# Kernel tuning notes

Measured on AMD Instinct MI355X. Metric: run time of the kernel, lower is better.

The kernel has to match this reference:

```python
import jax, jax.numpy as jnp
import numpy as np

B, N = 8, 2000                  # images, proposals per image
NUM_CLASSES = 91                # incl. background (class 0)
IMG_H, IMG_W = 800, 1333
SCORE_THRESH = 0.05
NMS_THRESH = 0.5
DETS_PER_IMG = 100
PRE_NMS_TOPK = 2048             # fixed-size cap on NMS candidates (jit-static)
MIN_SIZE = 0.01
WX, WY, WW, WH = 10.0, 10.0, 5.0, 5.0   # BoxCoder weights
BBOX_XFORM_CLIP = float(np.log(1000.0 / 16.0))


def setup_inputs() -> dict:
    key = jax.random.key(0)
    k1, k2, k3, k4 = jax.random.split(key, 4)
    # valid proposal boxes (x1,y1,x2,y2) inside the image
    ctr = jax.random.uniform(k1, (B, N, 2)) * jnp.array([IMG_W, IMG_H], jnp.float32)
    wh = jax.random.uniform(k2, (B, N, 2), minval=8.0, maxval=256.0)
    proposals = jnp.concatenate([ctr - 0.5 * wh, ctr + 0.5 * wh], axis=-1)
    class_logits = jax.random.normal(k3, (B * N, NUM_CLASSES)) * 2.0
    box_regression = jax.random.normal(k4, (B * N, NUM_CLASSES * 4)) * 0.2
    return {"class_logits": class_logits, "box_regression": box_regression,
            "proposals": proposals}


def _decode(reg, boxes):
    # reg: [N, C, 4] deltas, boxes: [N, 4] proposals -> [N, C, 4] decoded
    w = boxes[:, 2] - boxes[:, 0]
    h = boxes[:, 3] - boxes[:, 1]
    cx = boxes[:, 0] + 0.5 * w
    cy = boxes[:, 1] + 0.5 * h
    dx = reg[..., 0] / WX
    dy = reg[..., 1] / WY
    dw = jnp.minimum(reg[..., 2] / WW, BBOX_XFORM_CLIP)
    dh = jnp.minimum(reg[..., 3] / WH, BBOX_XFORM_CLIP)
    pcx = dx * w[:, None] + cx[:, None]
    pcy = dy * h[:, None] + cy[:, None]
    pw = jnp.exp(dw) * w[:, None]
    ph = jnp.exp(dh) * h[:, None]
    return jnp.stack([pcx - 0.5 * pw, pcy - 0.5 * ph,
                      pcx + 0.5 * pw, pcy + 0.5 * ph], axis=-1)


def _box_iou(a, b):
    # a: [K,4], b: [K,4] -> [K,K]
    area_a = (a[:, 2] - a[:, 0]) * (a[:, 3] - a[:, 1])
    area_b = (b[:, 2] - b[:, 0]) * (b[:, 3] - b[:, 1])
    lt = jnp.maximum(a[:, None, :2], b[None, :, :2])
    rb = jnp.minimum(a[:, None, 2:], b[None, :, 2:])
    wh = jnp.clip(rb - lt, 0.0)
    inter = wh[..., 0] * wh[..., 1]
    return inter / (area_a[:, None] + area_b[None, :] - inter)


def _postprocess_image(boxes, scores):
    # boxes: [N, C, 4] decoded, scores: [N, C] softmax probs
    boxes = jnp.stack([jnp.clip(boxes[..., 0], 0.0, IMG_W),
                       jnp.clip(boxes[..., 1], 0.0, IMG_H),
                       jnp.clip(boxes[..., 2], 0.0, IMG_W),
                       jnp.clip(boxes[..., 3], 0.0, IMG_H)], axis=-1)
    # drop background class 0, flatten to per-(proposal,class) candidates
    boxes_fg = boxes[:, 1:, :].reshape(-1, 4)            # [N*(C-1), 4]
    scores_fg = scores[:, 1:].reshape(-1)
    labels_fg = jnp.broadcast_to(jnp.arange(1, NUM_CLASSES, dtype=jnp.int32),
                                 (N, NUM_CLASSES - 1)).reshape(-1)
    ws = boxes_fg[:, 2] - boxes_fg[:, 0]
    hs = boxes_fg[:, 3] - boxes_fg[:, 1]
    valid = (scores_fg > SCORE_THRESH) & (ws >= MIN_SIZE) & (hs >= MIN_SIZE)
    # fixed-size pre-NMS top-K (masked-out candidates sorted last)
    _, top_idx = jax.lax.top_k(jnp.where(valid, scores_fg, -1.0), PRE_NMS_TOPK)
    cand_boxes = boxes_fg[top_idx]
    cand_scores = scores_fg[top_idx]
    cand_labels = labels_fg[top_idx]
    cand_valid = valid[top_idx]
    # class-wise (batched) NMS via per-class coordinate offset
    offset = cand_labels.astype(cand_boxes.dtype) * (jnp.max(cand_boxes) + 1.0)
    iou = _box_iou(cand_boxes + offset[:, None], cand_boxes + offset[:, None])
    idx = jnp.arange(PRE_NMS_TOPK)

    def body(i, keep):  # greedy suppression in score order
        sup = (iou[i] > NMS_THRESH) & keep[i] & (idx > i)
        return keep & ~sup

    keep = jax.lax.fori_loop(0, PRE_NMS_TOPK, body, cand_valid)
    out_scores, out_idx = jax.lax.top_k(jnp.where(keep, cand_scores, -1.0),
                                        DETS_PER_IMG)
    return cand_boxes[out_idx], out_scores, cand_labels[out_idx]


def reference(class_logits, box_regression, proposals):
    logits = class_logits.reshape(B, N, NUM_CLASSES)
    reg = box_regression.reshape(B, N, NUM_CLASSES, 4)
    pred_boxes = jax.vmap(_decode)(reg, proposals)          # [B, N, C, 4]
    pred_scores = jax.nn.softmax(logits, axis=-1)           # [B, N, C]
    boxes, scores, labels = jax.vmap(_postprocess_image)(pred_boxes, pred_scores)
    return boxes, scores, labels
```

## Files before the change

kernel.cpp:

```cpp
#include <hip/hip_runtime.h>
#include <cstdint>
#include <cstddef>

#define NIMG   8
#define NPROP  2000
#define NCLS   91
#define NFG    90
#define NROW   (NIMG * NPROP)
#define TOPK   2048
#define DETS   100
#define CKCAP  32768
#define KREGS  12
#define CLSCAP 512

#define IMG_Wf 1333.0f
#define IMG_Hf 800.0f
#define SCORE_TH 0.05f
#define MINSZ    0.01f
#define NMS_TH   0.5f
#define CLIPV    4.135166556742356f
#define ORD_NEG1 0x407FFFFFu
#define PADKEY   (((ull)ORD_NEG1 << 32) | 0xFFFFFFFFull)

typedef unsigned long long ull;

static const size_t OFF_CNT    = 0;
static const size_t OFF_VBM    = 4096;
static const size_t OFF_CK     = 262144;
static const size_t OFF_CBOX   = OFF_CK    + (size_t)NIMG*CKCAP*8;
static const size_t OFF_CSCOR  = OFF_CBOX  + (size_t)NIMG*TOPK*16;
static const size_t OFF_CLAB   = OFF_CSCOR + (size_t)NIMG*TOPK*4;
static const size_t OFF_CLSBOX = OFF_CLAB  + (size_t)NIMG*TOPK*4;
static const size_t OFF_CLSAR  = OFF_CLSBOX+ (size_t)NIMG*TOPK*16;
static const size_t OFF_CLSSX  = OFF_CLSAR + (size_t)NIMG*TOPK*4;
static const size_t OFF_CLSCNT = OFF_CLSSX + (size_t)NIMG*TOPK*4;
static const size_t OFF_CLSOFF = OFF_CLSCNT+ (size_t)NIMG*96*4;
static const size_t OFF_KCLS   = OFF_CLSOFF+ (size_t)NIMG*96*4;

__device__ __forceinline__ unsigned ford(float f) {
    unsigned u = __float_as_uint(f);
    return (u & 0x80000000u) ? ~u : (u | 0x80000000u);
}
__device__ __forceinline__ float fordinv(unsigned x) {
    return (x & 0x80000000u) ? __uint_as_float(x & 0x7FFFFFFFu)
                             : __uint_as_float(~x);
}

__device__ __forceinline__ float4 decode_clip(float4 p, float4 r) {
    float w  = __fsub_rn(p.z, p.x);
    float h  = __fsub_rn(p.w, p.y);
    float cx = __fadd_rn(p.x, __fmul_rn(0.5f, w));
    float cy = __fadd_rn(p.y, __fmul_rn(0.5f, h));
    float dx = __fdiv_rn(r.x, 10.0f);
    float dy = __fdiv_rn(r.y, 10.0f);
    float dw = fminf(__fdiv_rn(r.z, 5.0f), CLIPV);
    float dh = fminf(__fdiv_rn(r.w, 5.0f), CLIPV);
    float pcx = __fadd_rn(__fmul_rn(dx, w), cx);
    float pcy = __fadd_rn(__fmul_rn(dy, h), cy);
    float pw  = __fmul_rn(expf(dw), w);
    float ph  = __fmul_rn(expf(dh), h);
    float x1 = __fsub_rn(pcx, __fmul_rn(0.5f, pw));
    float y1 = __fsub_rn(pcy, __fmul_rn(0.5f, ph));
    float x2 = __fadd_rn(pcx, __fmul_rn(0.5f, pw));
    float y2 = __fadd_rn(pcy, __fmul_rn(0.5f, ph));
    float4 o;
    o.x = fminf(fmaxf(x1, 0.0f), IMG_Wf);
    o.y = fminf(fmaxf(y1, 0.0f), IMG_Hf);
    o.z = fminf(fmaxf(x2, 0.0f), IMG_Wf);
    o.w = fminf(fmaxf(y2, 0.0f), IMG_Hf);
    return o;
}

__device__ __forceinline__ void wl_phase(ull& a, ull& b, int l, int base,
                                         int k, int jmax) {
    bool desc = ((base & k) == 0);
    for (int j = jmax; j >= 2; j >>= 1) {
        int pl = l ^ (j >> 1);
        bool lower = ((base & j) == 0);
        ull pa = __shfl(a, pl), pb = __shfl(b, pl);
        bool km = (desc == lower);
        ull na = km ? (a > pa ? a : pa) : (a < pa ? a : pa);
        ull nb = km ? (b > pb ? b : pb) : (b < pb ? b : pb);
        a = na; b = nb;
    }
    ull mx = a > b ? a : b, mn = a > b ? b : a;
    a = desc ? mx : mn; b = desc ? mn : mx;
}

__global__ __launch_bounds__(1024) void kA(const float* __restrict__ logits,
                                           const float* __restrict__ reg,
                                           const float* __restrict__ props,
                                           ull* __restrict__ ck,
                                           int* __restrict__ cntv,
                                           ull* __restrict__ vbm2) {
    int warp = threadIdx.x >> 6;
    int lane = threadIdx.x & 63;
    int row  = blockIdx.x * 16 + warp;
    int b = row / NPROP;
    int n = row - b * NPROP;
    const float* lrow = logits + (size_t)row * NCLS;

    float xa = lrow[lane];
    float xb = (lane < 27) ? lrow[64 + lane] : -INFINITY;
    float mx = fmaxf(xa, xb);
    #pragma unroll
    for (int o = 32; o; o >>= 1) mx = fmaxf(mx, __shfl_xor(mx, o));
    float ea = expf(__fsub_rn(xa, mx));
    float eb = (lane < 27) ? expf(__fsub_rn(xb, mx)) : 0.0f;
    float s  = __fadd_rn(ea, eb);
    #pragma unroll
    for (int o = 32; o; o >>= 1) s = __fadd_rn(s, __shfl_xor(s, o));

    const float4 p = *reinterpret_cast<const float4*>(props + (size_t)row * 4);

    __shared__ int sCnt[32];
    __shared__ int sExc[32];
    __shared__ int sBase;

    ull rowmask[2];
    bool validA[2];
    ull keyA[2];
    #pragma unroll
    for (int it = 0; it < 2; ++it) {
        int c = (it == 0) ? (1 + lane) : (65 + lane);
        bool active = (it == 0) ? true : (lane < 26);
        bool valid = false;
        ull key = 0;
        if (active) {
            float lg = lrow[c];
            float score = __fdiv_rn(expf(__fsub_rn(lg, mx)), s);
            float4 r4 = *reinterpret_cast<const float4*>(
                reg + ((size_t)row * NCLS + c) * 4);
            float4 bx = decode_clip(p, r4);
            float bw = __fsub_rn(bx.z, bx.x);
            float bh = __fsub_rn(bx.w, bx.y);
            valid = (score > SCORE_TH) && (bw >= MINSZ) && (bh >= MINSZ);
            int offidx = n * NFG + (c - 1);
            key = ((ull)ford(score) << 32) |
                  (ull)(0xFFFFFFFFu - (unsigned)offidx);
        }
        ull bal = __ballot(valid);
        rowmask[it] = bal;
        validA[it] = valid;
        keyA[it] = key;
        if (lane == 0) sCnt[warp * 2 + it] = __popcll(bal);
    }
    __syncthreads();
    if (warp == 0) {
        int c = (lane < 32) ? sCnt[lane] : 0;
        int p2 = c;
        #pragma unroll
        for (int o = 1; o < 32; o <<= 1) {
            int v = __shfl_up(p2, o);
            if (lane >= o) p2 += v;
        }
        if (lane == 31) sBase = atomicAdd(&cntv[b * 64], p2);
        if (lane < 32) sExc[lane] = p2 - c;
    }
    __syncthreads();
    int base = sBase;
    #pragma unroll
    for (int it = 0; it < 2; ++it) {
        if (validA[it]) {
            int slot = base + sExc[warp * 2 + it] +
                       __popcll(rowmask[it] & ((1ull << lane) - 1ull));
            if (slot < CKCAP)
                ck[(size_t)b * CKCAP + slot] = keyA[it];
        }
    }
    if (lane == 0) {
        vbm2[(size_t)row * 2]     = rowmask[0];
        vbm2[(size_t)row * 2 + 1] = rowmask[1];
    }
}

__global__ __launch_bounds__(1024) void kB(const ull* __restrict__ ck,
                                           const int* __restrict__ cntv,
                                           const ull* __restrict__ vbm2,
                                           const float* __restrict__ reg,
                                           const float* __restrict__ props,
                                           float4* __restrict__ cbox,
                                           float* __restrict__ cscore,
                                           int* __restrict__ clabel,
                                           float4* __restrict__ clsbox,
                                           float* __restrict__ clsarea,
                                           int* __restrict__ clssidx,
                                           int* __restrict__ clscnt,
                                           int* __restrict__ clsoff) {
    int b = blockIdx.x;
    int tid = threadIdx.x;
    int lane = tid & 63, warp = tid >> 6;
    __shared__ ull sk[TOPK];
    __shared__ unsigned histw[16 * 256];
    __shared__ unsigned wtot4[4];
    __shared__ ull sP;
    __shared__ int sRem, sCnt, sDone;
    __shared__ float sMax[16];
    __shared__ float sM1;
    __shared__ int rex[NPROP];
    __shared__ int wsum[16];
    __shared__ ull clsbm[NFG * 33];
    __shared__ unsigned wpfx[NFG * 33];
    __shared__ int ccnt[96], coff[96];

    int cnt = cntv[b * 64];
    if (cnt > CKCAP) cnt = CKCAP;
    const ull* K = ck + (size_t)b * CKCAP;

    if (cnt >= TOPK) {
        ull kreg[KREGS];
        #pragma unroll
        for (int r = 0; r < KREGS; ++r) {
            int i = tid + (r << 10);
            kreg[r] = (i < cnt) ? K[i] : 0ull;
        }
        ull P = 0; int rem = TOPK;
        for (int pass = 7; pass >= 0; --pass) {
            int sh = pass * 8;
            *reinterpret_cast<uint4*>(&histw[tid * 4]) = make_uint4(0, 0, 0, 0);
            __syncthreads();
            ull pmask = (pass == 7) ? 0ull : (~0ull << (sh + 8));
            unsigned* hw = &histw[warp << 8];
            #pragma unroll
            for (int r = 0; r < KREGS; ++r) {
                int i = tid + (r << 10);
                if (i < cnt && (kreg[r] & pmask) == P)
                    atomicAdd(&hw[(unsigned)(kreg[r] >> sh) & 255u], 1u);
            }
            for (int i = (KREGS << 10) + tid; i < cnt; i += 1024) {
                ull k2 = K[i];
                if ((k2 & pmask) == P)
                    atomicAdd(&hw[(unsigned)(k2 >> sh) & 255u], 1u);
            }
            __syncthreads();
            unsigned x = 0, pfx = 0;
            if (tid < 256) {
                int d = 255 - tid;
                #pragma unroll
                for (int w = 0; w < 16; ++w) x += histw[(w << 8) + d];
                pfx = x;
                #pragma unroll
                for (int o = 1; o < 64; o <<= 1) {
                    unsigned v = __shfl_up(pfx, o);
                    if (lane >= o) pfx += v;
                }
                if (lane == 63) wtot4[tid >> 6] = pfx;
            }
            __syncthreads();
            if (tid < 256) {
                int d = 255 - tid;
                int ws = tid >> 6;
                unsigned add = 0;
                if (ws > 0) add += wtot4[0];
                if (ws > 1) add += wtot4[1];
                if (ws > 2) add += wtot4[2];
                unsigned pi   = pfx + add;
                unsigned excl = pi - x;
                if (x && excl < (unsigned)rem && pi >= (unsigned)rem) {
                    sP = P | ((ull)(unsigned)d << sh);
                    int nr = rem - (int)excl;
                    sRem = nr;
                    sDone = ((int)x == nr) ? 1 : 0;
                }
            }
            __syncthreads();
            P = sP; rem = sRem;
            if (sDone) break;
        }
        if (tid == 0) sCnt = 0;
        __syncthreads();
        #pragma unroll
        for (int r = 0; r < KREGS; ++r) {
            int i = tid + (r << 10);
            bool sel = (i < cnt) && (kreg[r] >= P);
            ull bal = __ballot(sel);
            int cw = __popcll(bal);
            if (cw) {
                int ldr = __ffsll((long long)bal) - 1;
                int bw = 0;
                if (lane == ldr) bw = atomicAdd(&sCnt, cw);
                bw = __shfl(bw, ldr);
                if (sel) {
                    int pos = bw + __popcll(bal & ((1ull << lane) - 1ull));
                    if (pos < TOPK) sk[pos] = kreg[r];
                }
            }
        }
        for (int i = (KREGS << 10) + tid; i < cnt; i += 1024) {
            ull k2 = K[i];
            bool sel = (k2 >= P);
            ull bal = __ballot(sel);
            int cw = __popcll(bal);
            if (cw) {
                int ldr = __ffsll((long long)bal) - 1;
                int bw = 0;
                if (lane == ldr) bw = atomicAdd(&sCnt, cw);
                bw = __shfl(bw, ldr);
                if (sel) {
                    int pos = bw + __popcll(bal & ((1ull << lane) - 1ull));
                    if (pos < TOPK) sk[pos] = k2;
                }
            }
        }
        __syncthreads();
        int fc = sCnt;
        for (int i = fc + tid; i < TOPK; i += 1024) sk[i] = PADKEY;
    } else {
        for (int i = tid; i < cnt; i += 1024) sk[i] = K[i];
        int F = TOPK - cnt;
        const ull* V = vbm2 + (size_t)b * NPROP * 2;
        int r0 = 2 * tid, r1 = r0 + 1;
        int v0 = 0, v1 = 0;
        if (r0 < NPROP) v0 = NFG - __popcll(V[r0 * 2]) - __popcll(V[r0 * 2 + 1]);
        if (r1 < NPROP) v1 = NFG - __popcll(V[r1 * 2]) - __popcll(V[r1 * 2 + 1]);
        int s2 = v0 + v1;
        int pfx = s2;
        #pragma unroll
        for (int o = 1; o < 64; o <<= 1) {
            int t = __shfl_up(pfx, o);
            if (lane >= o) pfx += t;
        }
        if (lane == 63) wsum[warp] = pfx;
        __syncthreads();
        if (tid == 0) {
            int a = 0;
            for (int w = 0; w < 16; ++w) { int t = wsum[w]; wsum[w] = a; a += t; }
        }
        __syncthreads();
        int excl = pfx - s2 + wsum[warp];
        if (r0 < NPROP) rex[r0] = excl;
        if (r1 < NPROP) rex[r1] = excl + v0;
        __syncthreads();
        for (int r = tid; r < NPROP; r += 1024) {
            int e = rex[r];
            if (e < F) {
                ull m0 = V[r * 2], m1 = V[r * 2 + 1];
                int rank = e;
                ull inv = ~m0;
                while (inv && rank < F) {
                    int cb = __builtin_ctzll(inv); inv &= inv - 1;
                    unsigned idx = (unsigned)(r * NFG + cb);
                    sk[cnt + rank] = ((ull)ORD_NEG1 << 32) | (ull)(0xFFFFFFFFu - idx);
                    ++rank;
                }
                inv = (~m1) & ((1ull << 26) - 1ull);
                while (inv && rank < F) {
                    int cb = __builtin_ctzll(inv); inv &= inv - 1;
                    unsigned idx = (unsigned)(r * NFG + 64 + cb);
                    sk[cnt + rank] = ((ull)ORD_NEG1 << 32) | (ull)(0xFFFFFFFFu - idx);
                    ++rank;
                }
            }
        }
    }
    __syncthreads();

    {
        int ebase = warp * 128 + lane * 2;
        ulonglong2 v = *reinterpret_cast<ulonglong2*>(&sk[ebase]);
        ull a = v.x, bb = v.y;
        #pragma unroll
        for (int k = 2; k <= 128; k <<= 1)
            wl_phase(a, bb, lane, ebase, k, (k >> 1) < 64 ? (k >> 1) : 64);
        v.x = a; v.y = bb;
        *reinterpret_cast<ulonglong2*>(&sk[ebase]) = v;
        for (int k = 256; k <= TOPK; k <<= 1) {
            for (int j = k >> 1; j >= 128; j >>= 1) {
                __syncthreads();
                int i = ((tid & ~(j - 1)) << 1) | (tid & (j - 1));
                int ij = i | j;
                ull x1 = sk[i], x2 = sk[ij];
                bool descSeg = ((i & k) == 0);
                if ((x1 < x2) == descSeg) { sk[i] = x2; sk[ij] = x1; }
            }
            __syncthreads();
            v = *reinterpret_cast<ulonglong2*>(&sk[ebase]);
            a = v.x; bb = v.y;
            wl_phase(a, bb, lane, ebase, k, 64);
            v.x = a; v.y = bb;
            *reinterpret_cast<ulonglong2*>(&sk[ebase]) = v;
        }
    }
    __syncthreads();

    float lmax = 0.0f;
    float4 myb[2]; int myl[2]; float mys[2]; bool vkA[2];
    #pragma unroll
    for (int r = 0; r < 2; ++r) {
        int sidx = tid + r * 1024;
        ull k = sk[sidx];
        unsigned idx = 0xFFFFFFFFu - (unsigned)(k & 0xFFFFFFFFu);
        float score = fordinv((unsigned)(k >> 32));
        int n = (int)(idx / NFG), c = (int)(idx % NFG);
        int row = b * NPROP + n;
        float4 p  = *reinterpret_cast<const float4*>(props + (size_t)row * 4);
        float4 r4 = *reinterpret_cast<const float4*>(
            reg + ((size_t)row * NCLS + (c + 1)) * 4);
        float4 bx = decode_clip(p, r4);
        myb[r] = bx; myl[r] = c + 1; mys[r] = score;
        vkA[r] = (((unsigned)(k >> 32)) != ORD_NEG1);
        lmax = fmaxf(lmax, fmaxf(fmaxf(bx.x, bx.y), fmaxf(bx.z, bx.w)));
    }
    #pragma unroll
    for (int o = 32; o; o >>= 1) lmax = fmaxf(lmax, __shfl_xor(lmax, o));
    if ((tid & 63) == 0) sMax[tid >> 6] = lmax;
    __syncthreads();
    if (tid == 0) {
        float v = sMax[0];
        for (int i = 1; i < 16; ++i) v = fmaxf(v, sMax[i]);
        sM1 = __fadd_rn(v, 1.0f);
    }
    __syncthreads();
    float m1 = sM1;
    float4 obA[2]; float arA[2];
    #pragma unroll
    for (int r = 0; r < 2; ++r) {
        int sidx = tid + r * 1024;
        float off = __fmul_rn((float)myl[r], m1);
        float4 ob;
        ob.x = __fadd_rn(myb[r].x, off);
        ob.y = __fadd_rn(myb[r].y, off);
        ob.z = __fadd_rn(myb[r].z, off);
        ob.w = __fadd_rn(myb[r].w, off);
        float area = __fmul_rn(__fsub_rn(ob.z, ob.x), __fsub_rn(ob.w, ob.y));
        obA[r] = ob; arA[r] = area;
        int g = b * TOPK + sidx;
        cbox[g] = myb[r]; cscore[g] = mys[r]; clabel[g] = myl[r];
    }

    for (int i = tid; i < NFG * 33; i += 1024) clsbm[i] = 0ull;
    __syncthreads();
    #pragma unroll
    for (int r = 0; r < 2; ++r) {
        int sidx = tid + (r << 10);
        if (vkA[r])
            atomicOr(&clsbm[(myl[r] - 1) * 33 + (sidx >> 6)], 1ull << (sidx & 63));
    }
    __syncthreads();
    if (tid < NFG) {
        unsigned run = 0;
        for (int w = 0; w < 32; ++w) {
            wpfx[tid * 33 + w] = run;
            run += (unsigned)__popcll(clsbm[tid * 33 + w]);
        }
        ccnt[tid] = (int)run;
    }
    __syncthreads();
    if (tid == 0) {
        int a = 0;
        for (int c2 = 0; c2 < NFG; ++c2) { coff[c2] = a; a += ccnt[c2]; }
    }
    __syncthreads();
    #pragma unroll
    for (int r = 0; r < 2; ++r) {
        int sidx = tid + (r << 10);
        if (vkA[r]) {
            int cl = myl[r] - 1;
            int rank = (int)wpfx[cl * 33 + (sidx >> 6)] +
                       (int)__popcll(clsbm[cl * 33 + (sidx >> 6)] &
                                     ((1ull << (sidx & 63)) - 1ull));
            int slot = coff[cl] + rank;
            int g2 = b * TOPK + slot;
            clsbox[g2] = obA[r]; clsarea[g2] = arA[r]; clssidx[g2] = sidx;
        }
    }
    if (tid < NFG) {
        clscnt[b * 96 + tid] = ccnt[tid];
        clsoff[b * 96 + tid] = coff[tid];
    }
}

__global__ __launch_bounds__(64) void kN(const float4* __restrict__ clsbox,
                                         const float* __restrict__ clsarea,
                                         const int* __restrict__ clscnt,
                                         const int* __restrict__ clsoff,
                                         ull* __restrict__ keepcls) {
    int bc = blockIdx.x;
    int b = bc / NFG, c = bc - b * NFG;
    int n = clscnt[b * 96 + c];
    if (n <= 0) return;
    if (n > CLSCAP) n = CLSCAP;
    int lane = threadIdx.x;
    int base = b * TOPK + clsoff[b * 96 + c];

    if (n <= 64) {
        float4 b0; float a0 = 0.0f;
        if (lane < n) {
            b0 = clsbox[base + lane];
            a0 = clsarea[base + lane];
        }
        ull alive = (n == 64) ? ~0ull : ((1ull << n) - 1ull);
        #pragma unroll 1
        for (int i = 0; i < n; ++i) {
            if (!((alive >> i) & 1ull)) continue;
            float bix = __shfl(b0.x, i), biy = __shfl(b0.y, i);
            float biz = __shfl(b0.z, i), biw = __shfl(b0.w, i);
            float ai2 = __shfl(a0, i);
            bool sup = false;
            if (lane < n && lane > i) {
                float lt0 = fmaxf(bix, b0.x), lt1 = fmaxf(biy, b0.y);
                float rb0 = fminf(biz, b0.z), rb1 = fminf(biw, b0.w);
                float w0 = fmaxf(__fsub_rn(rb0, lt0), 0.0f);
                float w1 = fmaxf(__fsub_rn(rb1, lt1), 0.0f);
                float inter = __fmul_rn(w0, w1);
                if (inter > 0.0f) {
                    float un = __fsub_rn(__fadd_rn(ai2, a0), inter);
                    sup = (__fdiv_rn(inter, un) > NMS_TH);
                }
            }
            alive &= ~__ballot(sup);
        }
        if (lane == 0) keepcls[(size_t)(b * 96 + c) * 8] = alive;
        return;
    }

    int W = (n + 63) >> 6;
    __shared__ float4 sbox[CLSCAP];
    __shared__ float  sar[CLSCAP];
    __shared__ ull    smask[CLSCAP * 8];
    for (int t = lane; t < n; t += 64) {
        sbox[t] = clsbox[base + t];
        sar[t]  = clsarea[base + t];
    }
    __syncthreads();
    for (int i = lane; i < n; i += 64) {
        float4 a = sbox[i]; float ai = sar[i];
        for (int w = 0; w < W; ++w) {
            ull word = 0;
            int jn = n - (w << 6); if (jn > 64) jn = 64;
            for (int s = 0; s < jn; ++s) {
                int j = (w << 6) + s;
                if (j > i) {
                    float4 cc = sbox[j];
                    float lt0 = fmaxf(a.x, cc.x), lt1 = fmaxf(a.y, cc.y);
                    float rb0 = fminf(a.z, cc.z), rb1 = fminf(a.w, cc.w);
                    float w0 = fmaxf(__fsub_rn(rb0, lt0), 0.0f);
                    float w1 = fmaxf(__fsub_rn(rb1, lt1), 0.0f);
                    float inter = __fmul_rn(w0, w1);
                    if (inter > 0.0f) {
                        float un = __fsub_rn(__fadd_rn(ai, sar[j]), inter);
                        if (__fdiv_rn(inter, un) > NMS_TH) word |= (1ull << s);
                    }
                }
            }
            smask[i * W + w] = word;
        }
    }
    __syncthreads();
    ull alive = 0;
    if (lane < W) {
        int rem = n - (lane << 6);
        alive = (rem >= 64) ? ~0ull : ((1ull << rem) - 1ull);
    }
    for (int i = 0; i < n; ++i) {
        ull aw = __shfl(alive, i >> 6);
        if ((aw >> (i & 63)) & 1ull) {
            if (lane < W) alive &= ~smask[i * W + lane];
        }
    }
    if (lane < W) keepcls[(size_t)(b * 96 + c) * 8 + lane] = alive;
}

__global__ __launch_bounds__(64) void kE(const ull* __restrict__ keepcls,
                                         const int* __restrict__ clssidx,
                                         const int* __restrict__ clscnt,
                                         const int* __restrict__ clsoff,
                                         const float4* __restrict__ cbox,
                                         const float* __restrict__ cscore,
                                         const int* __restrict__ clabel,
                                         float* __restrict__ out) {
    int b = blockIdx.x;
    int lane = threadIdx.x;
    __shared__ ull sKeep[32];
    if (lane < 32) sKeep[lane] = 0ull;
    __syncthreads();

    for (int c = lane; c < NFG; c += 64) {
        int n = clscnt[b * 96 + c];
        if (n <= 0) continue;
        if (n > CLSCAP) n = CLSCAP;
        int W = (n + 63) >> 6;
        int base = b * TOPK + clsoff[b * 96 + c];
        for (int w = 0; w < W; ++w) {
            ull bits = keepcls[(size_t)(b * 96 + c) * 8 + w];
            while (bits) {
                int s = __builtin_ctzll(bits); bits &= bits - 1;
                int sidx = clssidx[base + (w << 6) + s];
                atomicOr(&sKeep[sidx >> 6], 1ull << (sidx & 63));
            }
        }
    }
    __syncthreads();

    unsigned m = (unsigned)(sKeep[lane >> 1] >> ((lane & 1) << 5));

    int cntk = __popc(m);
    int pre = cntk;
    #pragma unroll
    for (int o = 1; o < 64; o <<= 1) {
        int v = __shfl_up(pre, o);
        if (lane >= o) pre += v;
    }
    int total = __shfl(pre, 63);
    int excl = pre - cntk;

    unsigned mm = m;
    while (mm) {
        int t = __builtin_ctz(mm);
        mm &= mm - 1;
        int rank = excl++;
        if (rank < DETS) {
            int j = lane * 32 + t;
            int g = b * TOPK + j;
            float4 bx = cbox[g];
            *reinterpret_cast<float4*>(out + ((size_t)b * DETS + rank) * 4) = bx;
            out[NIMG * DETS * 4 + b * DETS + rank] = cscore[g];
            out[NIMG * DETS * 5 + b * DETS + rank] = (float)clabel[g];
        }
    }
    int kept100 = (total < DETS) ? total : DETS;
    int F = DETS - kept100;
    if (F > 0) {
        unsigned zm = ~m;
        int zc = __popc(zm);
        int zpre = zc;
        #pragma unroll
        for (int o = 1; o < 64; o <<= 1) {
            int v = __shfl_up(zpre, o);
            if (lane >= o) zpre += v;
        }
        int zexcl = zpre - zc;
        while (zm) {
            int t = __builtin_ctz(zm);
            zm &= zm - 1;
            int zr = zexcl++;
            if (zr < F) {
                int j = lane * 32 + t;
                int g = b * TOPK + j;
                float4 bx = cbox[g];
                int rank = kept100 + zr;
                *reinterpret_cast<float4*>(out + ((size_t)b * DETS + rank) * 4) = bx;
                out[NIMG * DETS * 4 + b * DETS + rank] = -1.0f;
                out[NIMG * DETS * 5 + b * DETS + rank] = (float)clabel[g];
            }
        }
    }
}

extern "C" void kernel_launch(void* const* d_in, const int* in_sizes, int n_in,
                              void* d_out, int out_size, void* d_ws, size_t ws_size,
                              hipStream_t stream) {
    const float* logits = (const float*)d_in[0];
    const float* reg    = (const float*)d_in[1];
    const float* props  = (const float*)d_in[2];
    float* out = (float*)d_out;
    char* ws = (char*)d_ws;

    int* cntv   = (int*)(ws + OFF_CNT);
    ull* vbm2   = (ull*)(ws + OFF_VBM);
    ull* ck     = (ull*)(ws + OFF_CK);
    float4* cbox   = (float4*)(ws + OFF_CBOX);
    float*  cscor  = (float*)(ws + OFF_CSCOR);
    int*    clab   = (int*)(ws + OFF_CLAB);
    float4* clsbox = (float4*)(ws + OFF_CLSBOX);
    float*  clsar  = (float*)(ws + OFF_CLSAR);
    int*    clssx  = (int*)(ws + OFF_CLSSX);
    int*    clscnt = (int*)(ws + OFF_CLSCNT);
    int*    clsoff = (int*)(ws + OFF_CLSOFF);
    ull*    keepcls= (ull*)(ws + OFF_KCLS);

    hipMemsetAsync(ws, 0, 2048, stream);
    hipLaunchKernelGGL(kA, dim3(NROW / 16), dim3(1024), 0, stream,
                       logits, reg, props, ck, cntv, vbm2);
    hipLaunchKernelGGL(kB, dim3(NIMG), dim3(1024), 0, stream,
                       ck, cntv, vbm2, reg, props, cbox, cscor, clab,
                       clsbox, clsar, clssx, clscnt, clsoff);
    hipLaunchKernelGGL(kN, dim3(NIMG * NFG), dim3(64), 0, stream,
                       clsbox, clsar, clscnt, clsoff, keepcls);
    hipLaunchKernelGGL(kE, dim3(NIMG), dim3(64), 0, stream,
                       keepcls, clssx, clscnt, clsoff, cbox, cscor, clab, out);
}
```

Baseline: 139.8 us.

## Replace full 2048-key bitonic sort with per-class sorts and top-100 select

The full bitonic sort of the 2048 candidate keys in kB is removed, and candidates are scattered unsorted into per-class buckets through atomic slot allocation. Each kN block now sorts its own class bucket: a shuffle bitonic sort when the class has at most 64 entries, otherwise a serial selection sort in shared memory. NMS then writes per-candidate keep flags. kE is rewritten to radix-select the top 100 kept keys (then suppressed keys as filler) and bitonic-sort those 128 entries in one wave. This avoids sorting all 2048 entries in a single block per image, at the cost of an O(n²) selection sort for large classes and a more complex emit kernel.

After: 128.1 us. 8.4% less time.

```diff
diff --git a/kernel.cpp b/kernel.cpp
--- a/kernel.cpp
+++ b/kernel.cpp
@@ -32,10 +32,10 @@
 static const size_t OFF_CLAB   = OFF_CSCOR + (size_t)NIMG*TOPK*4;
 static const size_t OFF_CLSBOX = OFF_CLAB  + (size_t)NIMG*TOPK*4;
 static const size_t OFF_CLSAR  = OFF_CLSBOX+ (size_t)NIMG*TOPK*16;
-static const size_t OFF_CLSSX  = OFF_CLSAR + (size_t)NIMG*TOPK*4;
-static const size_t OFF_CLSCNT = OFF_CLSSX + (size_t)NIMG*TOPK*4;
+static const size_t OFF_CLSKEY = OFF_CLSAR + (size_t)NIMG*TOPK*4;
+static const size_t OFF_KEEPF  = OFF_CLSKEY+ (size_t)NIMG*TOPK*8;
+static const size_t OFF_CLSCNT = OFF_KEEPF + (size_t)NIMG*TOPK*4;
 static const size_t OFF_CLSOFF = OFF_CLSCNT+ (size_t)NIMG*96*4;
-static const size_t OFF_KCLS   = OFF_CLSOFF+ (size_t)NIMG*96*4;
 
 __device__ __forceinline__ unsigned ford(float f) {
     unsigned u = __float_as_uint(f);
@@ -71,20 +71,22 @@
     return o;
 }
 
-__device__ __forceinline__ void wl_phase(ull& a, ull& b, int l, int base,
-                                         int k, int jmax) {
+__device__ __forceinline__ void wl_pair(ull& a, ull& b, int& pa, int& pb,
+                                        int l, int base, int k, int jmax) {
     bool desc = ((base & k) == 0);
     for (int j = jmax; j >= 2; j >>= 1) {
         int pl = l ^ (j >> 1);
         bool lower = ((base & j) == 0);
-        ull pa = __shfl(a, pl), pb = __shfl(b, pl);
+        ull qa = __shfl(a, pl), qb = __shfl(b, pl);
+        int ra = __shfl(pa, pl), rb = __shfl(pb, pl);
         bool km = (desc == lower);
-        ull na = km ? (a > pa ? a : pa) : (a < pa ? a : pa);
-        ull nb = km ? (b > pb ? b : pb) : (b < pb ? b : pb);
-        a = na; b = nb;
-    }
-    ull mx = a > b ? a : b, mn = a > b ? b : a;
-    a = desc ? mx : mn; b = desc ? mn : mx;
+        bool ta = km ? (a > qa) : (a < qa);
+        a = ta ? a : qa;  pa = ta ? pa : ra;
+        bool tb = km ? (b > qb) : (b < qb);
+        b = tb ? b : qb;  pb = tb ? pb : rb;
+    }
+    bool sw = ((a < b) == desc);
+    if (sw) { ull t = a; a = b; b = t; int tp = pa; pa = pb; pb = tp; }
 }
 
 __global__ __launch_bounds__(1024) void kA(const float* __restrict__ logits,
@@ -184,7 +186,8 @@
                                            int* __restrict__ clabel,
                                            float4* __restrict__ clsbox,
                                            float* __restrict__ clsarea,
-                                           int* __restrict__ clssidx,
+                                           ull* __restrict__ clskey,
+                                           int* __restrict__ keepflag,
                                            int* __restrict__ clscnt,
                                            int* __restrict__ clsoff) {
     int b = blockIdx.x;
@@ -194,14 +197,12 @@
     __shared__ unsigned histw[16 * 256];
     __shared__ unsigned wtot4[4];
     __shared__ ull sP;
-    __shared__ int sRem, sCnt, sDone;
+    __shared__ int sRem, sCnt, sDone, sInv, sVT;
     __shared__ float sMax[16];
     __shared__ float sM1;
     __shared__ int rex[NPROP];
     __shared__ int wsum[16];
-    __shared__ ull clsbm[NFG * 33];
-    __shared__ unsigned wpfx[NFG * 33];
-    __shared__ int ccnt[96], coff[96];
+    __shared__ int ccnt[96], cplc[96], coff[96];
 
     int cnt = cntv[b * 64];
     if (cnt > CKCAP) cnt = CKCAP;
@@ -355,40 +356,12 @@
     }
     __syncthreads();
 
-    {
-        int ebase = warp * 128 + lane * 2;
-        ulonglong2 v = *reinterpret_cast<ulonglong2*>(&sk[ebase]);
-        ull a = v.x, bb = v.y;
-        #pragma unroll
-        for (int k = 2; k <= 128; k <<= 1)
-            wl_phase(a, bb, lane, ebase, k, (k >> 1) < 64 ? (k >> 1) : 64);
-        v.x = a; v.y = bb;
-        *reinterpret_cast<ulonglong2*>(&sk[ebase]) = v;
-        for (int k = 256; k <= TOPK; k <<= 1) {
-            for (int j = k >> 1; j >= 128; j >>= 1) {
-                __syncthreads();
-                int i = ((tid & ~(j - 1)) << 1) | (tid & (j - 1));
-                int ij = i | j;
-                ull x1 = sk[i], x2 = sk[ij];
-                bool descSeg = ((i & k) == 0);
-                if ((x1 < x2) == descSeg) { sk[i] = x2; sk[ij] = x1; }
-            }
-            __syncthreads();
-            v = *reinterpret_cast<ulonglong2*>(&sk[ebase]);
-            a = v.x; bb = v.y;
-            wl_phase(a, bb, lane, ebase, k, 64);
-            v.x = a; v.y = bb;
-            *reinterpret_cast<ulonglong2*>(&sk[ebase]) = v;
-        }
-    }
-    __syncthreads();
-
     float lmax = 0.0f;
-    float4 myb[2]; int myl[2]; float mys[2]; bool vkA[2];
+    float4 myb[2]; int myl[2]; float mys[2]; bool vkA[2]; ull kkA[2];
     #pragma unroll
     for (int r = 0; r < 2; ++r) {
-        int sidx = tid + r * 1024;
-        ull k = sk[sidx];
+        int pos0 = tid + r * 1024;
+        ull k = sk[pos0];
         unsigned idx = 0xFFFFFFFFu - (unsigned)(k & 0xFFFFFFFFu);
         float score = fordinv((unsigned)(k >> 32));
         int n = (int)(idx / NFG), c = (int)(idx % NFG);
@@ -397,25 +370,43 @@
         float4 r4 = *reinterpret_cast<const float4*>(
             reg + ((size_t)row * NCLS + (c + 1)) * 4);
         float4 bx = decode_clip(p, r4);
-        myb[r] = bx; myl[r] = c + 1; mys[r] = score;
+        myb[r] = bx; myl[r] = c + 1; mys[r] = score; kkA[r] = k;
         vkA[r] = (((unsigned)(k >> 32)) != ORD_NEG1);
         lmax = fmaxf(lmax, fmaxf(fmaxf(bx.x, bx.y), fmaxf(bx.z, bx.w)));
     }
     #pragma unroll
     for (int o = 32; o; o >>= 1) lmax = fmaxf(lmax, __shfl_xor(lmax, o));
     if ((tid & 63) == 0) sMax[tid >> 6] = lmax;
+    if (tid < 96) { ccnt[tid] = 0; cplc[tid] = 0; }
+    if (tid == 0) sInv = 0;
     __syncthreads();
     if (tid == 0) {
         float v = sMax[0];
         for (int i = 1; i < 16; ++i) v = fmaxf(v, sMax[i]);
         sM1 = __fadd_rn(v, 1.0f);
     }
+    #pragma unroll
+    for (int r = 0; r < 2; ++r)
+        if (vkA[r]) atomicAdd(&ccnt[myl[r] - 1], 1);
+    __syncthreads();
+    if (tid == 0) {
+        int a = 0;
+        for (int c2 = 0; c2 < NFG; ++c2) { coff[c2] = a; a += ccnt[c2]; }
+        sVT = a;
+    }
     __syncthreads();
     float m1 = sM1;
-    float4 obA[2]; float arA[2];
+    int validTot = sVT;
     #pragma unroll
     for (int r = 0; r < 2; ++r) {
-        int sidx = tid + r * 1024;
+        int slot;
+        if (vkA[r]) {
+            int cl = myl[r] - 1;
+            slot = coff[cl] + atomicAdd(&cplc[cl], 1);
+        } else {
+            slot = validTot + atomicAdd(&sInv, 1);
+        }
+        int g2 = b * TOPK + slot;
         float off = __fmul_rn((float)myl[r], m1);
         float4 ob;
         ob.x = __fadd_rn(myb[r].x, off);
@@ -423,46 +414,9 @@
         ob.z = __fadd_rn(myb[r].z, off);
         ob.w = __fadd_rn(myb[r].w, off);
         float area = __fmul_rn(__fsub_rn(ob.z, ob.x), __fsub_rn(ob.w, ob.y));
-        obA[r] = ob; arA[r] = area;
-        int g = b * TOPK + sidx;
-        cbox[g] = myb[r]; cscore[g] = mys[r]; clabel[g] = myl[r];
-    }
-
-    for (int i = tid; i < NFG * 33; i += 1024) clsbm[i] = 0ull;
-    __syncthreads();
-    #pragma unroll
-    for (int r = 0; r < 2; ++r) {
-        int sidx = tid + (r << 10);
-        if (vkA[r])
-            atomicOr(&clsbm[(myl[r] - 1) * 33 + (sidx >> 6)], 1ull << (sidx & 63));
-    }
-    __syncthreads();
-    if (tid < NFG) {
-        unsigned run = 0;
-        for (int w = 0; w < 32; ++w) {
-            wpfx[tid * 33 + w] = run;
-            run += (unsigned)__popcll(clsbm[tid * 33 + w]);
-        }
-        ccnt[tid] = (int)run;
-    }
-    __syncthreads();
-    if (tid == 0) {
-        int a = 0;
-        for (int c2 = 0; c2 < NFG; ++c2) { coff[c2] = a; a += ccnt[c2]; }
-    }
-    __syncthreads();
-    #pragma unroll
-    for (int r = 0; r < 2; ++r) {
-        int sidx = tid + (r << 10);
-        if (vkA[r]) {
-            int cl = myl[r] - 1;
-            int rank = (int)wpfx[cl * 33 + (sidx >> 6)] +
-                       (int)__popcll(clsbm[cl * 33 + (sidx >> 6)] &
-                                     ((1ull << (sidx & 63)) - 1ull));
-            int slot = coff[cl] + rank;
-            int g2 = b * TOPK + slot;
-            clsbox[g2] = obA[r]; clsarea[g2] = arA[r]; clssidx[g2] = sidx;
-        }
+        clsbox[g2] = ob; clsarea[g2] = area; clskey[g2] = kkA[r];
+        cbox[g2] = myb[r]; cscore[g2] = mys[r]; clabel[g2] = myl[r];
+        keepflag[g2] = 0;
     }
     if (tid < NFG) {
         clscnt[b * 96 + tid] = ccnt[tid];
@@ -472,9 +426,10 @@
 
 __global__ __launch_bounds__(64) void kN(const float4* __restrict__ clsbox,
                                          const float* __restrict__ clsarea,
+                                         const ull* __restrict__ clskey,
                                          const int* __restrict__ clscnt,
                                          const int* __restrict__ clsoff,
-                                         ull* __restrict__ keepcls) {
+                                         int* __restrict__ keepflag) {
     int bc = blockIdx.x;
     int b = bc / NFG, c = bc - b * NFG;
     int n = clscnt[b * 96 + c];
@@ -484,11 +439,25 @@
     int base = b * TOPK + clsoff[b * 96 + c];
 
     if (n <= 64) {
+        ull key = (lane < n) ? clskey[base + lane] : (ull)lane;
+        int slot = (lane < n) ? (base + lane) : -1;
+        #pragma unroll
+        for (int k = 2; k <= 64; k <<= 1) {
+            #pragma unroll
+            for (int j = k >> 1; j > 0; j >>= 1) {
+                int pl = lane ^ j;
+                ull qk = __shfl(key, pl);
+                int qs = __shfl(slot, pl);
+                bool desc = ((lane & k) == 0);
+                bool lower = ((lane & j) == 0);
+                bool km = (desc == lower);
+                bool keepown = km ? (key > qk) : (key < qk);
+                key = keepown ? key : qk;
+                slot = keepown ? slot : qs;
+            }
+        }
         float4 b0; float a0 = 0.0f;
-        if (lane < n) {
-            b0 = clsbox[base + lane];
-            a0 = clsarea[base + lane];
-        }
+        if (slot >= 0) { b0 = clsbox[slot]; a0 = clsarea[slot]; }
         ull alive = (n == 64) ? ~0ull : ((1ull << n) - 1ull);
         #pragma unroll 1
         for (int i = 0; i < n; ++i) {
@@ -510,19 +479,43 @@
             }
             alive &= ~__ballot(sup);
         }
-        if (lane == 0) keepcls[(size_t)(b * 96 + c) * 8] = alive;
+        if (lane < n) keepflag[slot] = (int)((alive >> lane) & 1ull);
         return;
     }
 
-    int W = (n + 63) >> 6;
+    __shared__ ull  skey[CLSCAP];
+    __shared__ int  sslot[CLSCAP];
     __shared__ float4 sbox[CLSCAP];
     __shared__ float  sar[CLSCAP];
     __shared__ ull    smask[CLSCAP * 8];
+    __shared__ ull    salive[8];
     for (int t = lane; t < n; t += 64) {
-        sbox[t] = clsbox[base + t];
-        sar[t]  = clsarea[base + t];
-    }
-    __syncthreads();
+        skey[t] = clskey[base + t];
+        sslot[t] = base + t;
+    }
+    __syncthreads();
+    for (int r = 0; r < n - 1; ++r) {
+        ull best = 0; int bi = -1;
+        for (int t = r + lane; t < n; t += 64)
+            if (skey[t] > best) { best = skey[t]; bi = t; }
+        #pragma unroll
+        for (int o = 32; o; o >>= 1) {
+            ull ob = __shfl_xor(best, o);
+            int oi = __shfl_xor(bi, o);
+            if (ob > best) { best = ob; bi = oi; }
+        }
+        if (lane == 0 && bi != r) {
+            ull tk = skey[r]; skey[r] = skey[bi]; skey[bi] = tk;
+            int ts = sslot[r]; sslot[r] = sslot[bi]; sslot[bi] = ts;
+        }
+        __syncthreads();
+    }
+    for (int t = lane; t < n; t += 64) {
+        sbox[t] = clsbox[sslot[t]];
+        sar[t]  = clsarea[sslot[t]];
+    }
+    __syncthreads();
+    int W = (n + 63) >> 6;
     for (int i = lane; i < n; i += 64) {
         float4 a = sbox[i]; float ai = sar[i];
         for (int w = 0; w < W; ++w) {
@@ -558,92 +551,162 @@
             if (lane < W) alive &= ~smask[i * W + lane];
         }
     }
-    if (lane < W) keepcls[(size_t)(b * 96 + c) * 8 + lane] = alive;
-}
-
-__global__ __launch_bounds__(64) void kE(const ull* __restrict__ keepcls,
-                                         const int* __restrict__ clssidx,
-                                         const int* __restrict__ clscnt,
-                                         const int* __restrict__ clsoff,
-                                         const float4* __restrict__ cbox,
-                                         const float* __restrict__ cscore,
-                                         const int* __restrict__ clabel,
-                                         float* __restrict__ out) {
+    if (lane < W) salive[lane] = alive;
+    __syncthreads();
+    for (int t = lane; t < n; t += 64)
+        keepflag[sslot[t]] = (int)((salive[t >> 6] >> (t & 63)) & 1ull);
+}
+
+__global__ __launch_bounds__(1024) void kE(const int* __restrict__ keepflag,
+                                           const ull* __restrict__ clskey,
+                                           const float4* __restrict__ cbox,
+                                           const float* __restrict__ cscore,
+                                           const int* __restrict__ clabel,
+                                           float* __restrict__ out) {
     int b = blockIdx.x;
-    int lane = threadIdx.x;
-    __shared__ ull sKeep[32];
-    if (lane < 32) sKeep[lane] = 0ull;
-    __syncthreads();
-
-    for (int c = lane; c < NFG; c += 64) {
-        int n = clscnt[b * 96 + c];
-        if (n <= 0) continue;
-        if (n > CLSCAP) n = CLSCAP;
-        int W = (n + 63) >> 6;
-        int base = b * TOPK + clsoff[b * 96 + c];
-        for (int w = 0; w < W; ++w) {
-            ull bits = keepcls[(size_t)(b * 96 + c) * 8 + w];
-            while (bits) {
-                int s = __builtin_ctzll(bits); bits &= bits - 1;
-                int sidx = clssidx[base + (w << 6) + s];
-                atomicOr(&sKeep[sidx >> 6], 1ull << (sidx & 63));
-            }
-        }
-    }
-    __syncthreads();
-
-    unsigned m = (unsigned)(sKeep[lane >> 1] >> ((lane & 1) << 5));
-
-    int cntk = __popc(m);
-    int pre = cntk;
-    #pragma unroll
-    for (int o = 1; o < 64; o <<= 1) {
-        int v = __shfl_up(pre, o);
-        if (lane >= o) pre += v;
-    }
-    int total = __shfl(pre, 63);
-    int excl = pre - cntk;
-
-    unsigned mm = m;
-    while (mm) {
-        int t = __builtin_ctz(mm);
-        mm &= mm - 1;
-        int rank = excl++;
-        if (rank < DETS) {
-            int j = lane * 32 + t;
-            int g = b * TOPK + j;
-            float4 bx = cbox[g];
-            *reinterpret_cast<float4*>(out + ((size_t)b * DETS + rank) * 4) = bx;
-            out[NIMG * DETS * 4 + b * DETS + rank] = cscore[g];
-            out[NIMG * DETS * 5 + b * DETS + rank] = (float)clabel[g];
-        }
-    }
-    int kept100 = (total < DETS) ? total : DETS;
-    int F = DETS - kept100;
-    if (F > 0) {
-        unsigned zm = ~m;
-        int zc = __popc(zm);
-        int zpre = zc;
-        #pragma unroll
-        for (int o = 1; o < 64; o <<= 1) {
-            int v = __shfl_up(zpre, o);
-            if (lane >= o) zpre += v;
-        }
-        int zexcl = zpre - zc;
-        while (zm) {
-            int t = __builtin_ctz(zm);
-            zm &= zm - 1;
-            int zr = zexcl++;
-            if (zr < F) {
-                int j = lane * 32 + t;
-                int g = b * TOPK + j;
-                float4 bx = cbox[g];
-                int rank = kept100 + zr;
-                *reinterpret_cast<float4*>(out + ((size_t)b * DETS + rank) * 4) = bx;
-                out[NIMG * DETS * 4 + b * DETS + rank] = -1.0f;
-                out[NIMG * DETS * 5 + b * DETS + rank] = (float)clabel[g];
-            }
-        }
+    int tid = threadIdx.x;
+    int lane = tid & 63, warp = tid >> 6;
+    __shared__ ull kk[TOPK];
+    __shared__ int ks[TOPK];
+    __shared__ unsigned histw[16 * 256];
+    __shared__ unsigned wtot4[4];
+    __shared__ ull sP;
+    __shared__ int sRem, sDone, sK, sFC;
+    __shared__ ull fkey[128];
+    __shared__ int fslot[128];
+
+    const ull* KY = clskey + (size_t)b * TOPK;
+    const int* KF = keepflag + (size_t)b * TOPK;
+
+    int emitted = 0;
+    #pragma unroll 1
+    for (int seg = 0; seg < 2; ++seg) {
+        __syncthreads();
+        if (tid == 0) sK = 0;
+        __syncthreads();
+        if (emitted < DETS) {
+            for (int s = tid; s < TOPK; s += 1024) {
+                bool f = (seg == 0) ? (KF[s] != 0) : (KF[s] == 0);
+                ull key = KY[s];
+                ull bal = __ballot(f);
+                int cw = __popcll(bal);
+                if (cw) {
+                    int ldr = __ffsll((long long)bal) - 1;
+                    int bw = 0;
+                    if (lane == ldr) bw = atomicAdd(&sK, cw);
+                    bw = __shfl(bw, ldr);
+                    if (f) {
+                        int p = bw + __popcll(bal & ((1ull << lane) - 1ull));
+                        kk[p] = key; ks[p] = s;
+                    }
+                }
+            }
+        }
+        __syncthreads();
+        int K = sK;
+        int T = DETS - emitted;
+        if (T > K) T = K;
+        if (emitted < DETS && K > 0) {
+            ull P = 0;
+            if (K > T) {
+                int rem = T;
+                for (int pass = 7; pass >= 0; --pass) {
+                    int sh = pass * 8;
+                    *reinterpret_cast<uint4*>(&histw[tid * 4]) = make_uint4(0, 0, 0, 0);
+                    __syncthreads();
+                    ull pmask = (pass == 7) ? 0ull : (~0ull << (sh + 8));
+                    unsigned* hw = &histw[warp << 8];
+                    for (int i = tid; i < K; i += 1024) {
+                        ull k2 = kk[i];
+                        if ((k2 & pmask) == P)
+                            atomicAdd(&hw[(unsigned)(k2 >> sh) & 255u], 1u);
+                    }
+                    __syncthreads();
+                    unsigned x = 0, pfx = 0;
+                    if (tid < 256) {
+                        int d = 255 - tid;
+                        #pragma unroll
+                        for (int w = 0; w < 16; ++w) x += histw[(w << 8) + d];
+                        pfx = x;
+                        #pragma unroll
+                        for (int o = 1; o < 64; o <<= 1) {
+                            unsigned v = __shfl_up(pfx, o);
+                            if (lane >= o) pfx += v;
+                        }
+                        if (lane == 63) wtot4[tid >> 6] = pfx;
+                    }
+                    __syncthreads();
+                    if (tid < 256) {
+                        int d = 255 - tid;
+                        int ws = tid >> 6;
+                        unsigned add = 0;
+                        if (ws > 0) add += wtot4[0];
+                        if (ws > 1) add += wtot4[1];
+                        if (ws > 2) add += wtot4[2];
+                        unsigned pi   = pfx + add;
+                        unsigned excl = pi - x;
+                        if (x && excl < (unsigned)rem && pi >= (unsigned)rem) {
+                            sP = P | ((ull)(unsigned)d << sh);
+                            int nr = rem - (int)excl;
+                            sRem = nr;
+                            sDone = ((int)x == nr) ? 1 : 0;
+                        }
+                    }
+                    __syncthreads();
+                    P = sP; rem = sRem;
+                    if (sDone) break;
+                }
+            }
+            if (tid == 0) sFC = 0;
+            __syncthreads();
+            for (int i = tid; i < K; i += 1024) {
+                ull k2 = kk[i];
+                bool sel = (k2 >= P);
+                ull bal = __ballot(sel);
+                int cw = __popcll(bal);
+                if (cw) {
+                    int ldr = __ffsll((long long)bal) - 1;
+                    int bw = 0;
+                    if (lane == ldr) bw = atomicAdd(&sFC, cw);
+                    bw = __shfl(bw, ldr);
+                    if (sel) {
+                        int p2 = bw + __popcll(bal & ((1ull << lane) - 1ull));
+                        if (p2 < T) { fkey[p2] = k2; fslot[p2] = ks[i]; }
+                    }
+                }
+            }
+            __syncthreads();
+            int FC = sFC; if (FC > T) FC = T;
+            for (int i = FC + tid; i < 128; i += 1024) { fkey[i] = 0; fslot[i] = -1; }
+            __syncthreads();
+            if (warp == 0) {
+                int base2 = lane * 2;
+                ull a = fkey[base2], bb = fkey[base2 + 1];
+                int pa = fslot[base2], pb = fslot[base2 + 1];
+                #pragma unroll
+                for (int k = 2; k <= 128; k <<= 1)
+                    wl_pair(a, bb, pa, pb, lane, base2, k,
+                            (k >> 1) < 64 ? (k >> 1) : 64);
+                #pragma unroll
+                for (int e = 0; e < 2; ++e) {
+                    int rnk = base2 + e;
+                    ull kv = e ? bb : a;
+                    int sl = e ? pb : pa;
+                    (void)kv;
+                    if (rnk < T && sl >= 0) {
+                        int r2 = emitted + rnk;
+                        int g = b * TOPK + sl;
+                        float4 bx = cbox[g];
+                        *reinterpret_cast<float4*>(out + ((size_t)b * DETS + r2) * 4) = bx;
+                        out[NIMG * DETS * 4 + b * DETS + r2] =
+                            (seg == 0) ? cscore[g] : -1.0f;
+                        out[NIMG * DETS * 5 + b * DETS + r2] = (float)clabel[g];
+                    }
+                }
+            }
+            emitted += T;
+        }
+        __syncthreads();
     }
 }
 
@@ -664,19 +727,19 @@
     int*    clab   = (int*)(ws + OFF_CLAB);
     float4* clsbox = (float4*)(ws + OFF_CLSBOX);
     float*  clsar  = (float*)(ws + OFF_CLSAR);
-    int*    clssx  = (int*)(ws + OFF_CLSSX);
+    ull*    clskey = (ull*)(ws + OFF_CLSKEY);
+    int*    keepf  = (int*)(ws + OFF_KEEPF);
     int*    clscnt = (int*)(ws + OFF_CLSCNT);
     int*    clsoff = (int*)(ws + OFF_CLSOFF);
-    ull*    keepcls= (ull*)(ws + OFF_KCLS);
 
     hipMemsetAsync(ws, 0, 2048, stream);
     hipLaunchKernelGGL(kA, dim3(NROW / 16), dim3(1024), 0, stream,
                        logits, reg, props, ck, cntv, vbm2);
     hipLaunchKernelGGL(kB, dim3(NIMG), dim3(1024), 0, stream,
                        ck, cntv, vbm2, reg, props, cbox, cscor, clab,
-                       clsbox, clsar, clssx, clscnt, clsoff);
+                       clsbox, clsar, clskey, keepf, clscnt, clsoff);
     hipLaunchKernelGGL(kN, dim3(NIMG * NFG), dim3(64), 0, stream,
-                       clsbox, clsar, clscnt, clsoff, keepcls);
-    hipLaunchKernelGGL(kE, dim3(NIMG), dim3(64), 0, stream,
-                       keepcls, clssx, clscnt, clsoff, cbox, cscor, clab, out);
-}
+                       clsbox, clsar, clskey, clscnt, clsoff, keepf);
+    hipLaunchKernelGGL(kE, dim3(NIMG), dim3(1024), 0, stream,
+                       keepf, clskey, cbox, cscor, clab, out);
+}
```
